# Optimization experiments

Measured on AMD Instinct MI355X. Metric: run time of the kernel, lower is better.

The kernel has to match this reference:

```python
import jax, jax.numpy as jnp
import numpy as np

SIZE = (128.0, 128.0, 128.0)
FEATURE_BLOCK_IDS = (1, 2, 3)


def _trilerp(feat, coords, power):
    # feat: [B, D, H, W, C]; coords: [B, N, 3] in [0, 1]
    B = coords.shape[0]
    scale = jnp.asarray([0.5 ** power * SIZE[0],
                         0.5 ** power * SIZE[1],
                         0.5 ** power * SIZE[2]], dtype=coords.dtype)
    hi = float(min(feat.shape[1:4])) - 1.01
    idx = jnp.clip(coords * scale, 0.01, hi)  # [B, N, 3]
    ix, iy, iz = idx[..., 0], idx[..., 1], idx[..., 2]
    x1, x2 = jnp.floor(ix), jnp.ceil(ix)
    y1, y2 = jnp.floor(iy), jnp.ceil(iy)
    z1, z2 = jnp.floor(iz), jnp.ceil(iz)
    b = jnp.arange(B)[:, None]  # broadcast batch index

    def g(xi, yi, zi):
        return feat[b, xi.astype(jnp.int32), yi.astype(jnp.int32), zi.astype(jnp.int32)]

    wx, wx2 = (ix - x1)[..., None], (x2 - ix)[..., None]
    wy, wy2 = (iy - y1)[..., None], (y2 - iy)[..., None]
    wz, wz2 = (iz - z1)[..., None], (z2 - iz)[..., None]

    # z = z1 plane
    lerp_x1 = g(x2, y1, z1) * wx + g(x1, y1, z1) * wx2
    lerp_x2 = g(x2, y2, z1) * wx + g(x1, y2, z1) * wx2
    lerp_y1 = lerp_x2 * wy + lerp_x1 * wy2
    # z = z2 plane
    lerp_x1 = g(x2, y1, z2) * wx + g(x1, y1, z2) * wx2
    lerp_x2 = g(x2, y2, z2) * wx + g(x1, y2, z2) * wx2
    lerp_y2 = lerp_x2 * wy + lerp_x1 * wy2
    return lerp_y2 * wz + lerp_y1 * wz2  # [B, N, C]


def setup_inputs() -> dict:
    key = jax.random.key(0)
    ks = jax.random.split(key, 7)
    B, N = 2, 50000
    return {
        'features0': jax.random.normal(ks[0], (B, 128, 128, 128, 1), jnp.float32),
        'features1': jax.random.normal(ks[1], (B, 64, 64, 64, 32), jnp.float32),
        'features2': jax.random.normal(ks[2], (B, 32, 32, 32, 64), jnp.float32),
        'features3': jax.random.normal(ks[3], (B, 16, 16, 16, 128), jnp.float32),
        'features4': jax.random.normal(ks[4], (B, 8, 8, 8, 256), jnp.float32),
        'mesh_coords': jax.random.uniform(ks[5], (B, N, 3), jnp.float32),
        'mesh_features': jax.random.normal(ks[6], (B, N, 3), jnp.float32),
    }


def reference(features0, features1, features2, features3, features4, mesh_coords, mesh_features):
    feats = [features0, features1, features2, features3, features4]
    # mesh_coords is [B, N, 3] -> one coord group, reshape is identity
    sampled = [_trilerp(feats[i], mesh_coords, i) for i in FEATURE_BLOCK_IDS]
    out = jnp.concatenate(sampled, axis=-1)
    return jnp.concatenate([out, mesh_features], axis=-1)
```

## Files before the change

### kernel.cpp

```cpp
#include <hip/hip_runtime.h>


typedef float floatx4 __attribute__((ext_vector_type(4)));

__device__ __forceinline__ int point_batch(int p, int N) {
    int b = 0;
    while (p >= N) { p -= N; ++b; }
    return b;
}

template<int D, int LPP, int OCB>
__device__ __forceinline__ void do_level(const float* __restrict__ fbase,
                                         const float* __restrict__ coords,
                                         float* __restrict__ out,
                                         int pBase, int N, int P)
{
    const int tid  = threadIdx.x;
    const int lane = tid & 63;
    const int wv   = tid >> 6;
    const int p    = pBase + wv * (64 / LPP) + (lane / LPP);
    const int c4   = lane & (LPP - 1);
    if (p >= P) return;

    const float cx = coords[p * 3 + 0];
    const float cy = coords[p * 3 + 1];
    const float cz = coords[p * 3 + 2];

    const float scale = (float)D;
    const float hi    = (float)((double)D - 1.01);

    const float ix = fminf(fmaxf(cx * scale, 0.01f), hi);
    const float iy = fminf(fmaxf(cy * scale, 0.01f), hi);
    const float iz = fminf(fmaxf(cz * scale, 0.01f), hi);

    const float x1f = floorf(ix), x2f = ceilf(ix);
    const float y1f = floorf(iy), y2f = ceilf(iy);
    const float z1f = floorf(iz), z2f = ceilf(iz);
    const int x1 = (int)x1f, x2 = (int)x2f;
    const int y1 = (int)y1f, y2 = (int)y2f;
    const int z1 = (int)z1f, z2 = (int)z2f;

    const float wx = ix - x1f, wx2 = x2f - ix;
    const float wy = iy - y1f, wy2 = y2f - iy;
    const float wz = iz - z1f, wz2 = z2f - iz;

    const unsigned baseB = (unsigned)point_batch(p, N) * (unsigned)(D * D * D * LPP * 16)
                         + (unsigned)c4 * 16u;
    #define OFFB(X, Y, Z) (baseB + (unsigned)((((X) * D + (Y)) * D + (Z)) * LPP) * 16u)

    floatx4 v111, v211, v121, v221, v112, v212, v122, v222;
    asm volatile("global_load_dwordx4 %0, %1, %2"
                 : "=v"(v111) : "v"(OFFB(x1, y1, z1)), "s"(fbase));
    asm volatile("global_load_dwordx4 %0, %1, %2"
                 : "=v"(v211) : "v"(OFFB(x2, y1, z1)), "s"(fbase));
    asm volatile("global_load_dwordx4 %0, %1, %2"
                 : "=v"(v121) : "v"(OFFB(x1, y2, z1)), "s"(fbase));
    asm volatile("global_load_dwordx4 %0, %1, %2"
                 : "=v"(v221) : "v"(OFFB(x2, y2, z1)), "s"(fbase));
    asm volatile("global_load_dwordx4 %0, %1, %2"
                 : "=v"(v112) : "v"(OFFB(x1, y1, z2)), "s"(fbase));
    asm volatile("global_load_dwordx4 %0, %1, %2"
                 : "=v"(v212) : "v"(OFFB(x2, y1, z2)), "s"(fbase));
    asm volatile("global_load_dwordx4 %0, %1, %2"
                 : "=v"(v122) : "v"(OFFB(x1, y2, z2)), "s"(fbase));
    asm volatile("global_load_dwordx4 %0, %1, %2"
                 : "=v"(v222) : "v"(OFFB(x2, y2, z2)), "s"(fbase));
    #undef OFFB

    asm volatile("s_waitcnt vmcnt(0)");
    __builtin_amdgcn_sched_barrier(0);

    const floatx4 lx1a = v211 * wx + v111 * wx2;
    const floatx4 lx2a = v221 * wx + v121 * wx2;
    const floatx4 ly1  = lx2a * wy + lx1a * wy2;
    const floatx4 lx1b = v212 * wx + v112 * wx2;
    const floatx4 lx2b = v222 * wx + v122 * wx2;
    const floatx4 ly2  = lx2b * wy + lx1b * wy2;
    const floatx4 r    = ly2  * wz + ly1  * wz2;

    float* o = out + p * 227 + OCB + c4 * 4;
    __builtin_nontemporal_store(r.x, o + 0);
    __builtin_nontemporal_store(r.y, o + 1);
    __builtin_nontemporal_store(r.z, o + 2);
    __builtin_nontemporal_store(r.w, o + 3);
}

__global__ __launch_bounds__(256, 8) void trilerp_kernel(
    const float* __restrict__ f1,
    const float* __restrict__ f2,
    const float* __restrict__ f3,
    const float* __restrict__ coords,
    const float* __restrict__ meshf,
    float* __restrict__ out,
    int N, int P, int nb1, int nb2, int nb3)
{
    const int blk = blockIdx.x;
    if (blk < nb1) {
        do_level<64, 8, 0>(f1, coords, out, blk * 32, N, P);
    } else if (blk < nb1 + nb2) {
        do_level<32, 16, 32>(f2, coords, out, (blk - nb1) * 16, N, P);
    } else if (blk < nb1 + nb2 + nb3) {
        do_level<16, 32, 96>(f3, coords, out, (blk - nb1 - nb2) * 8, N, P);
    } else {
        const int e = (blk - nb1 - nb2 - nb3) * 256 + (int)threadIdx.x;
        if (e < P * 3) {
            const int p = e / 3, c = e - p * 3;
            __builtin_nontemporal_store(meshf[e], &out[p * 227 + 224 + c]);
        }
    }
}

extern "C" void kernel_launch(void* const* d_in, const int* in_sizes, int n_in,
                              void* d_out, int out_size, void* d_ws, size_t ws_size,
                              hipStream_t stream) {
    const float* f1     = (const float*)d_in[1];
    const float* f2     = (const float*)d_in[2];
    const float* f3     = (const float*)d_in[3];
    const float* coords = (const float*)d_in[5];
    const float* meshf  = (const float*)d_in[6];
    float* out = (float*)d_out;

    const int B = in_sizes[1] / (64 * 64 * 64 * 32);
    const int N = in_sizes[5] / (B * 3);
    const int P = B * N;

    const int nb1 = (P + 31) / 32;
    const int nb2 = (P + 15) / 16;
    const int nb3 = (P + 7) / 8;
    const int nbm = (P * 3 + 255) / 256;
    const int grid = nb1 + nb2 + nb3 + nbm;

    trilerp_kernel<<<dim3(grid), dim3(256), 0, stream>>>(
        f1, f2, f3, coords, meshf, out, N, P, nb1, nb2, nb3);
}
```

Measured before the change: 210.8 us.

## Bucket-sort points spatially and remap workgroups across XCDs for gather locality

Adds a counting sort (histogram, single-block scan, atomic scatter) that groups points into 16^3 spatial buckets per batch, and the trilinear gather kernel then processes points in that permuted order. It also remaps block IDs so consecutive logical blocks land on the same XCD, improving L2 reuse of neighbouring feature voxels. The intent is to cut scattered DRAM traffic from random gathers, at the cost of three extra small kernel launches, a memset, an indirection load, and output writes that become scattered rows.

```diff
diff --git a/kernel.cpp b/kernel.cpp
--- a/kernel.cpp
+++ b/kernel.cpp
@@ -9,18 +9,73 @@
     return b;
 }
 
+__device__ __forceinline__ int bucket_of(const float* __restrict__ coords,
+                                         int p, int N) {
+    const float cx = coords[p * 3 + 0];
+    const float cy = coords[p * 3 + 1];
+    const float cz = coords[p * 3 + 2];
+    int bx = (int)(cx * 16.0f); bx = bx < 0 ? 0 : (bx > 15 ? 15 : bx);
+    int by = (int)(cy * 16.0f); by = by < 0 ? 0 : (by > 15 ? 15 : by);
+    int bz = (int)(cz * 16.0f); bz = bz < 0 ? 0 : (bz > 15 ? 15 : bz);
+    return ((point_batch(p, N) * 16 + bx) * 16 + by) * 16 + bz;
+}
+
+__global__ __launch_bounds__(256) void hist_kernel(
+    const float* __restrict__ coords, unsigned* __restrict__ bins,
+    int N, int P)
+{
+    const int p = blockIdx.x * 256 + (int)threadIdx.x;
+    if (p < P) atomicAdd(&bins[bucket_of(coords, p, N)], 1u);
+}
+
+__global__ __launch_bounds__(1024) void scan_kernel(unsigned* __restrict__ bins)
+{
+    __shared__ unsigned part[1024];
+    const int t = threadIdx.x;
+    unsigned loc[8];
+    unsigned s = 0;
+    for (int i = 0; i < 8; ++i) {
+        unsigned v = bins[t * 8 + i];
+        loc[i] = s;
+        s += v;
+    }
+    part[t] = s;
+    __syncthreads();
+    for (int off = 1; off < 1024; off <<= 1) {
+        unsigned v = (t >= off) ? part[t - off] : 0u;
+        __syncthreads();
+        part[t] += v;
+        __syncthreads();
+    }
+    const unsigned base = (t == 0) ? 0u : part[t - 1];
+    for (int i = 0; i < 8; ++i) bins[t * 8 + i] = base + loc[i];
+}
+
+__global__ __launch_bounds__(256) void scatter_kernel(
+    const float* __restrict__ coords, unsigned* __restrict__ bins,
+    unsigned* __restrict__ perm, int N, int P)
+{
+    const int p = blockIdx.x * 256 + (int)threadIdx.x;
+    if (p < P) {
+        const unsigned pos = atomicAdd(&bins[bucket_of(coords, p, N)], 1u);
+        perm[pos] = (unsigned)p;
+    }
+}
+
 template<int D, int LPP, int OCB>
 __device__ __forceinline__ void do_level(const float* __restrict__ fbase,
                                          const float* __restrict__ coords,
+                                         const unsigned* __restrict__ perm,
                                          float* __restrict__ out,
-                                         int pBase, int N, int P)
+                                         int sBase, int N, int P)
 {
     const int tid  = threadIdx.x;
     const int lane = tid & 63;
     const int wv   = tid >> 6;
-    const int p    = pBase + wv * (64 / LPP) + (lane / LPP);
+    const int slot = sBase + wv * (64 / LPP) + (lane / LPP);
     const int c4   = lane & (LPP - 1);
-    if (p >= P) return;
+    if (slot >= P) return;
+    const int p = perm ? (int)perm[slot] : slot;
 
     const float cx = coords[p * 3 + 0];
     const float cy = coords[p * 3 + 1];
@@ -91,16 +146,22 @@
     const float* __restrict__ f3,
     const float* __restrict__ coords,
     const float* __restrict__ meshf,
+    const unsigned* __restrict__ perm,
     float* __restrict__ out,
     int N, int P, int nb1, int nb2, int nb3)
 {
-    const int blk = blockIdx.x;
+    const int nwg  = (int)gridDim.x;
+    const int orig = (int)blockIdx.x;
+    const int q = nwg >> 3, r = nwg & 7;
+    const int xcd = orig & 7, j = orig >> 3;
+    const int blk = (xcd < r ? xcd * (q + 1) : r * (q + 1) + (xcd - r) * q) + j;
+
     if (blk < nb1) {
-        do_level<64, 8, 0>(f1, coords, out, blk * 32, N, P);
+        do_level<64, 8, 0>(f1, coords, perm, out, blk * 32, N, P);
     } else if (blk < nb1 + nb2) {
-        do_level<32, 16, 32>(f2, coords, out, (blk - nb1) * 16, N, P);
+        do_level<32, 16, 32>(f2, coords, perm, out, (blk - nb1) * 16, N, P);
     } else if (blk < nb1 + nb2 + nb3) {
-        do_level<16, 32, 96>(f3, coords, out, (blk - nb1 - nb2) * 8, N, P);
+        do_level<16, 32, 96>(f3, coords, perm, out, (blk - nb1 - nb2) * 8, N, P);
     } else {
         const int e = (blk - nb1 - nb2 - nb3) * 256 + (int)threadIdx.x;
         if (e < P * 3) {
@@ -124,6 +185,20 @@
     const int N = in_sizes[5] / (B * 3);
     const int P = B * N;
 
+    const int NBINS = 8192;
+    const size_t ws_need = (size_t)NBINS * 4 + (size_t)P * 4;
+    unsigned* bins = (unsigned*)d_ws;
+    unsigned* perm = bins + NBINS;
+    const bool do_sort = (d_ws != nullptr) && (ws_size >= ws_need);
+
+    if (do_sort) {
+        hipMemsetAsync(bins, 0, NBINS * 4, stream);
+        const int nbp = (P + 255) / 256;
+        hist_kernel<<<dim3(nbp), dim3(256), 0, stream>>>(coords, bins, N, P);
+        scan_kernel<<<dim3(1), dim3(1024), 0, stream>>>(bins);
+        scatter_kernel<<<dim3(nbp), dim3(256), 0, stream>>>(coords, bins, perm, N, P);
+    }
+
     const int nb1 = (P + 31) / 32;
     const int nb2 = (P + 15) / 16;
     const int nb3 = (P + 7) / 8;
@@ -131,5 +206,6 @@
     const int grid = nb1 + nb2 + nb3 + nbm;
 
     trilerp_kernel<<<dim3(grid), dim3(256), 0, stream>>>(
-        f1, f2, f3, coords, meshf, out, N, P, nb1, nb2, nb3);
-}
+        f1, f2, f3, coords, meshf, do_sort ? perm : nullptr,
+        out, N, P, nb1, nb2, nb3);
+}
```

After: 255.9 us. +21.4%, slower.

## Fuse all levels per point into one block and stage rows in shared memory

Applied to the files above, without the earlier changes.

Each block now handles 4 points and covers all three feature levels plus the mesh features, with threads assigned roles by channel range. Results are assembled in a shared-memory row buffer and then written out as contiguous, fully coalesced 16-byte nontemporal stores over the 227-float rows, replacing the scattered per-level strided writes. Inline-asm loads become plain vector loads, and the batch index is now computed assuming B<=2. The cost is divergence between roles within a wave, a block barrier, and reduced parallelism per block, since only 236 of 256 threads work.

```diff
diff --git a/kernel.cpp b/kernel.cpp
--- a/kernel.cpp
+++ b/kernel.cpp
@@ -3,110 +3,98 @@
 
 typedef float floatx4 __attribute__((ext_vector_type(4)));
 
-__device__ __forceinline__ int point_batch(int p, int N) {
-    int b = 0;
-    while (p >= N) { p -= N; ++b; }
-    return b;
-}
+#define G 4
+#define THREADS 256
 
-template<int D, int LPP, int OCB>
-__device__ __forceinline__ void do_level(const float* __restrict__ fbase,
-                                         const float* __restrict__ coords,
-                                         float* __restrict__ out,
-                                         int pBase, int N, int P)
-{
-    const int tid  = threadIdx.x;
-    const int lane = tid & 63;
-    const int wv   = tid >> 6;
-    const int p    = pBase + wv * (64 / LPP) + (lane / LPP);
-    const int c4   = lane & (LPP - 1);
-    if (p >= P) return;
-
-    const float cx = coords[p * 3 + 0];
-    const float cy = coords[p * 3 + 1];
-    const float cz = coords[p * 3 + 2];
-
-    const float scale = (float)D;
-    const float hi    = (float)((double)D - 1.01);
-
-    const float ix = fminf(fmaxf(cx * scale, 0.01f), hi);
-    const float iy = fminf(fmaxf(cy * scale, 0.01f), hi);
-    const float iz = fminf(fmaxf(cz * scale, 0.01f), hi);
-
-    const float x1f = floorf(ix), x2f = ceilf(ix);
-    const float y1f = floorf(iy), y2f = ceilf(iy);
-    const float z1f = floorf(iz), z2f = ceilf(iz);
-    const int x1 = (int)x1f, x2 = (int)x2f;
-    const int y1 = (int)y1f, y2 = (int)y2f;
-    const int z1 = (int)z1f, z2 = (int)z2f;
-
-    const float wx = ix - x1f, wx2 = x2f - ix;
-    const float wy = iy - y1f, wy2 = y2f - iy;
-    const float wz = iz - z1f, wz2 = z2f - iz;
-
-    const unsigned baseB = (unsigned)point_batch(p, N) * (unsigned)(D * D * D * LPP * 16)
-                         + (unsigned)c4 * 16u;
-    #define OFFB(X, Y, Z) (baseB + (unsigned)((((X) * D + (Y)) * D + (Z)) * LPP) * 16u)
-
-    floatx4 v111, v211, v121, v221, v112, v212, v122, v222;
-    asm volatile("global_load_dwordx4 %0, %1, %2"
-                 : "=v"(v111) : "v"(OFFB(x1, y1, z1)), "s"(fbase));
-    asm volatile("global_load_dwordx4 %0, %1, %2"
-                 : "=v"(v211) : "v"(OFFB(x2, y1, z1)), "s"(fbase));
-    asm volatile("global_load_dwordx4 %0, %1, %2"
-                 : "=v"(v121) : "v"(OFFB(x1, y2, z1)), "s"(fbase));
-    asm volatile("global_load_dwordx4 %0, %1, %2"
-                 : "=v"(v221) : "v"(OFFB(x2, y2, z1)), "s"(fbase));
-    asm volatile("global_load_dwordx4 %0, %1, %2"
-                 : "=v"(v112) : "v"(OFFB(x1, y1, z2)), "s"(fbase));
-    asm volatile("global_load_dwordx4 %0, %1, %2"
-                 : "=v"(v212) : "v"(OFFB(x2, y1, z2)), "s"(fbase));
-    asm volatile("global_load_dwordx4 %0, %1, %2"
-                 : "=v"(v122) : "v"(OFFB(x1, y2, z2)), "s"(fbase));
-    asm volatile("global_load_dwordx4 %0, %1, %2"
-                 : "=v"(v222) : "v"(OFFB(x2, y2, z2)), "s"(fbase));
-    #undef OFFB
-
-    asm volatile("s_waitcnt vmcnt(0)");
-    __builtin_amdgcn_sched_barrier(0);
-
-    const floatx4 lx1a = v211 * wx + v111 * wx2;
-    const floatx4 lx2a = v221 * wx + v121 * wx2;
-    const floatx4 ly1  = lx2a * wy + lx1a * wy2;
-    const floatx4 lx1b = v212 * wx + v112 * wx2;
-    const floatx4 lx2b = v222 * wx + v122 * wx2;
-    const floatx4 ly2  = lx2b * wy + lx1b * wy2;
-    const floatx4 r    = ly2  * wz + ly1  * wz2;
-
-    float* o = out + p * 227 + OCB + c4 * 4;
-    __builtin_nontemporal_store(r.x, o + 0);
-    __builtin_nontemporal_store(r.y, o + 1);
-    __builtin_nontemporal_store(r.z, o + 2);
-    __builtin_nontemporal_store(r.w, o + 3);
-}
-
-__global__ __launch_bounds__(256, 8) void trilerp_kernel(
+__global__ __launch_bounds__(THREADS, 8) void trilerp_fused_kernel(
     const float* __restrict__ f1,
     const float* __restrict__ f2,
     const float* __restrict__ f3,
     const float* __restrict__ coords,
     const float* __restrict__ meshf,
     float* __restrict__ out,
-    int N, int P, int nb1, int nb2, int nb3)
+    int N, int P)
 {
-    const int blk = blockIdx.x;
-    if (blk < nb1) {
-        do_level<64, 8, 0>(f1, coords, out, blk * 32, N, P);
-    } else if (blk < nb1 + nb2) {
-        do_level<32, 16, 32>(f2, coords, out, (blk - nb1) * 16, N, P);
-    } else if (blk < nb1 + nb2 + nb3) {
-        do_level<16, 32, 96>(f3, coords, out, (blk - nb1 - nb2) * 8, N, P);
-    } else {
-        const int e = (blk - nb1 - nb2 - nb3) * 256 + (int)threadIdx.x;
-        if (e < P * 3) {
-            const int p = e / 3, c = e - p * 3;
-            __builtin_nontemporal_store(meshf[e], &out[p * 227 + 224 + c]);
+    __shared__ float rowbuf[G * 227];
+    const int tid = (int)threadIdx.x;
+    const int p0  = (int)blockIdx.x * G;
+
+    if (tid < G * 56) {
+        const int pt   = tid / 56;
+        const int role = tid - pt * 56;
+        const int p    = p0 + pt;
+        if (p < P) {
+            const int lvl = (role < 8) ? 0 : ((role < 24) ? 1 : 2);
+            const int D   = 64 >> lvl;
+            const int C   = 32 << lvl;
+            const int c4  = role - ((lvl == 0) ? 0 : ((lvl == 1) ? 8 : 24));
+            const int ocb = (lvl == 0) ? 0 : ((lvl == 1) ? 32 : 96);
+            const float* fb = (lvl == 0) ? f1 : ((lvl == 1) ? f2 : f3);
+
+            const int b = (p >= N) ? 1 : 0;
+
+            const float cx = coords[p * 3 + 0];
+            const float cy = coords[p * 3 + 1];
+            const float cz = coords[p * 3 + 2];
+
+            const float scale = (float)D;
+            const float hi    = (float)((double)D - 1.01);
+
+            const float ix = fminf(fmaxf(cx * scale, 0.01f), hi);
+            const float iy = fminf(fmaxf(cy * scale, 0.01f), hi);
+            const float iz = fminf(fmaxf(cz * scale, 0.01f), hi);
+
+            const float x1f = floorf(ix), x2f = ceilf(ix);
+            const float y1f = floorf(iy), y2f = ceilf(iy);
+            const float z1f = floorf(iz), z2f = ceilf(iz);
+            const int x1 = (int)x1f, x2 = (int)x2f;
+            const int y1 = (int)y1f, y2 = (int)y2f;
+            const int z1 = (int)z1f, z2 = (int)z2f;
+
+            const float wx = ix - x1f, wx2 = x2f - ix;
+            const float wy = iy - y1f, wy2 = y2f - iy;
+            const float wz = iz - z1f, wz2 = z2f - iz;
+
+            #define OFF(X, Y, Z) ((((((b) * D + (X)) * D + (Y)) * D + (Z)) * C) + c4 * 4)
+            const floatx4 v111 = *(const floatx4*)(fb + OFF(x1, y1, z1));
+            const floatx4 v211 = *(const floatx4*)(fb + OFF(x2, y1, z1));
+            const floatx4 v121 = *(const floatx4*)(fb + OFF(x1, y2, z1));
+            const floatx4 v221 = *(const floatx4*)(fb + OFF(x2, y2, z1));
+            const floatx4 v112 = *(const floatx4*)(fb + OFF(x1, y1, z2));
+            const floatx4 v212 = *(const floatx4*)(fb + OFF(x2, y1, z2));
+            const floatx4 v122 = *(const floatx4*)(fb + OFF(x1, y2, z2));
+            const floatx4 v222 = *(const floatx4*)(fb + OFF(x2, y2, z2));
+            #undef OFF
+
+            const floatx4 lx1a = v211 * wx + v111 * wx2;
+            const floatx4 lx2a = v221 * wx + v121 * wx2;
+            const floatx4 ly1v = lx2a * wy + lx1a * wy2;
+            const floatx4 lx1b = v212 * wx + v112 * wx2;
+            const floatx4 lx2b = v222 * wx + v122 * wx2;
+            const floatx4 ly2v = lx2b * wy + lx1b * wy2;
+            const floatx4 r    = ly2v * wz + ly1v * wz2;
+
+            float* rb = rowbuf + pt * 227 + ocb + c4 * 4;
+            rb[0] = r.x; rb[1] = r.y; rb[2] = r.z; rb[3] = r.w;
         }
+    } else if (tid < G * 56 + G * 3) {
+        const int i  = tid - G * 56;
+        const int pt = i / 3, c = i - pt * 3;
+        const int p  = p0 + pt;
+        if (p < P) rowbuf[pt * 227 + 224 + c] = meshf[p * 3 + c];
+    }
+
+    __syncthreads();
+
+    const int nrow = min(G, P - p0);
+    if (nrow == G) {
+        if (tid < 227) {
+            const floatx4 v = *(const floatx4*)(rowbuf + tid * 4);
+            __builtin_nontemporal_store(v, (floatx4*)(out + (size_t)p0 * 227) + tid);
+        }
+    } else if (nrow > 0) {
+        for (int i = tid; i < nrow * 227; i += THREADS)
+            out[(size_t)p0 * 227 + i] = rowbuf[i];
     }
 }
 
@@ -124,12 +112,7 @@
     const int N = in_sizes[5] / (B * 3);
     const int P = B * N;
 
-    const int nb1 = (P + 31) / 32;
-    const int nb2 = (P + 15) / 16;
-    const int nb3 = (P + 7) / 8;
-    const int nbm = (P * 3 + 255) / 256;
-    const int grid = nb1 + nb2 + nb3 + nbm;
-
-    trilerp_kernel<<<dim3(grid), dim3(256), 0, stream>>>(
-        f1, f2, f3, coords, meshf, out, N, P, nb1, nb2, nb3);
+    const int grid = (P + G - 1) / G;
+    trilerp_fused_kernel<<<dim3(grid), dim3(THREADS), 0, stream>>>(
+        f1, f2, f3, coords, meshf, out, N, P);
 }
```

Result: no change. 214.6 us (+1.8%).
